# Performance work log

Measured on AMD Instinct MI355X. Metric: run time of the kernel, lower is better.

Reference implementation:

```python
import jax, jax.numpy as jnp
from jax import lax
import numpy as np

NUM_GRIDS = (40, 36, 24, 16, 12)
B, C = 4, 256
SMPL_OUT, CATE_OUT = 157, 1  # 24*6 pose + 10 shape + 3 cam; num_classes-1
SIZES = ((200, 200), (100, 100), (50, 50), (25, 25), (13, 13))


def setup_inputs():
    key = jax.random.key(0)
    ks = jax.random.split(key, 16)
    inp = {}
    for i, (h, w) in enumerate(SIZES):
        inp['feat%d' % i] = jax.random.normal(ks[i], (B, C, h, w), jnp.float32)
    def W(k, shape):
        return jax.random.normal(k, shape, jnp.float32) * 0.02
    inp['smpl_w0'] = W(ks[5], (C, C + 2, 3, 3)); inp['smpl_b0'] = jnp.zeros((C,), jnp.float32)
    inp['smpl_w'] = W(ks[6], (3, C, C, 3, 3)); inp['smpl_b'] = jnp.zeros((3, C), jnp.float32)
    inp['cate_w0'] = W(ks[7], (C, C, 3, 3)); inp['cate_b0'] = jnp.zeros((C,), jnp.float32)
    inp['cate_w'] = W(ks[8], (3, C, C, 3, 3)); inp['cate_b'] = jnp.zeros((3, C), jnp.float32)
    inp['cate_head_w'] = W(ks[9], (CATE_OUT, C, 3, 3)); inp['cate_head_b'] = jnp.zeros((CATE_OUT,), jnp.float32)
    inp['smpl_head_w'] = W(ks[10], (SMPL_OUT, C, 1, 1)); inp['smpl_head_b'] = jnp.zeros((SMPL_OUT,), jnp.float32)
    inp['smpl_init'] = W(ks[11], (SMPL_OUT,))  # stands in for init_contrep/shape/cam buffer
    return inp


def conv2d(x, w, b, pad):
    y = lax.conv_general_dilated(x, w, (1, 1), [(pad, pad), (pad, pad)],
                                 dimension_numbers=('NCHW', 'OIHW', 'NCHW'))
    return y + b[None, :, None, None]


def resize_ac(x, oh, ow):
    # bilinear resize, align_corners=True (matches F.interpolate(..., align_corners=True))
    H, W = x.shape[-2], x.shape[-1]
    ys = jnp.linspace(0.0, H - 1.0, oh)
    xs = jnp.linspace(0.0, W - 1.0, ow)
    y0 = jnp.floor(ys).astype(jnp.int32); y1 = jnp.minimum(y0 + 1, H - 1)
    x0 = jnp.floor(xs).astype(jnp.int32); x1 = jnp.minimum(x0 + 1, W - 1)
    wy = (ys - y0)[:, None]; wx = xs - x0
    r0, r1 = x[..., y0, :], x[..., y1, :]
    top = r0[..., x0] * (1 - wx) + r0[..., x1] * wx
    bot = r1[..., x0] * (1 - wx) + r1[..., x1] * wx
    return top * (1 - wy) + bot * wy


def points_nms(heat):
    # max_pool2d(kernel=2, stride=1, pad=1) -> (H+1, W+1); compare on [:-1, :-1]
    hmax = lax.reduce_window(heat, -jnp.inf, lax.max, (1, 1, 2, 2), (1, 1, 1, 1),
                             [(0, 0), (0, 0), (1, 1), (1, 1)])[:, :, :-1, :-1]
    return heat * (hmax == heat).astype(heat.dtype)


def _forward(feats, p):
    # split_feats: downsample P2 by 0.5, upsample P6 to P5 size (both align_corners bilinear)
    f0 = resize_ac(feats[0], feats[0].shape[-2] // 2, feats[0].shape[-1] // 2)
    f4 = resize_ac(feats[4], feats[3].shape[-2], feats[3].shape[-1])
    new_feats = (f0, feats[1], feats[2], feats[3], f4)
    smpl_outs, cate_outs = [], []
    for idx, x in enumerate(new_feats):
        g = NUM_GRIDS[idx]
        b, _, h, w = x.shape
        xr = jnp.linspace(-1.0, 1.0, w); yr = jnp.linspace(-1.0, 1.0, h)
        yy, xx = jnp.meshgrid(yr, xr, indexing='ij')
        coord = jnp.broadcast_to(jnp.stack([xx, yy])[None], (b, 2, h, w))  # CoordConv
        smpl_feat = resize_ac(jnp.concatenate([x, coord], axis=1), g, g)
        cate_feat = resize_ac(x, g, g)
        smpl_feat = jax.nn.relu(conv2d(smpl_feat, p['smpl_w0'], p['smpl_b0'], 1))
        cate_feat = jax.nn.relu(conv2d(cate_feat, p['cate_w0'], p['cate_b0'], 1))
        for i in range(3):  # remaining stacked convs (weights shared across levels)
            smpl_feat = jax.nn.relu(conv2d(smpl_feat, p['smpl_w'][i], p['smpl_b'][i], 1))
            cate_feat = jax.nn.relu(conv2d(cate_feat, p['cate_w'][i], p['cate_b'][i], 1))
        cate_pred = conv2d(cate_feat, p['cate_head_w'], p['cate_head_b'], 1)
        smpl_pred = conv2d(smpl_feat, p['smpl_head_w'], p['smpl_head_b'], 0) \
                    + p['smpl_init'][None, :, None, None]
        # eval=True branch: points-NMS on sigmoid heatmap, NHWC permute
        cate_pred = points_nms(jax.nn.sigmoid(cate_pred)).transpose(0, 2, 3, 1)
        smpl_pred = smpl_pred.transpose(0, 2, 3, 1)
        smpl_outs.append(smpl_pred); cate_outs.append(cate_pred)
    return tuple(smpl_outs) + tuple(cate_outs)


def reference(feat0, feat1, feat2, feat3, feat4, smpl_w0, smpl_b0, smpl_w, smpl_b,
              cate_w0, cate_b0, cate_w, cate_b, cate_head_w, cate_head_b,
              smpl_head_w, smpl_head_b, smpl_init):
    p = dict(smpl_w0=smpl_w0, smpl_b0=smpl_b0, smpl_w=smpl_w, smpl_b=smpl_b,
             cate_w0=cate_w0, cate_b0=cate_b0, cate_w=cate_w, cate_b=cate_b,
             cate_head_w=cate_head_w, cate_head_b=cate_head_b,
             smpl_head_w=smpl_head_w, smpl_head_b=smpl_head_b, smpl_init=smpl_init)
    return _forward((feat0, feat1, feat2, feat3, feat4), p)
```

## Files before the change

kernel.cpp:

```cpp
#include <hip/hip_runtime.h>
#include <math.h>
#include <stdint.h>

#define NLEV 5
#define PPT 17616
#define HPX 320

typedef __attribute__((ext_vector_type(8))) __bf16 bf16x8;
typedef __attribute__((ext_vector_type(4))) float f32x4;
typedef unsigned int u32;
typedef unsigned short u16;

#define MFMA16 __builtin_amdgcn_mfma_f32_16x16x32_bf16

__device__ __forceinline__ u32 f2bf(float f) {
  u32 u = __builtin_bit_cast(u32, f);
  return (u + 0x7FFFu + ((u >> 16) & 1u)) >> 16;
}
__device__ __forceinline__ void split2(float v, u32& hi, u32& lo) {
  hi = f2bf(v);
  lo = f2bf(v - __builtin_bit_cast(float, hi << 16));
}
__device__ __forceinline__ float bf2f(u32 bits16) {
  return __builtin_bit_cast(float, bits16 << 16);
}


struct PrepDesc {
  const float* src[9];
  int Cin[9];
  int Cout[9];
  int CB[9];
  int TAPS[9];
  int nCoT[9];
  int dstOff[9];
};

__global__ __launch_bounds__(256) void prep_weights(PrepDesc pd, u16* __restrict__ wHi,
                                                    u16* __restrict__ wLo) {
  int cfg = blockIdx.y;
  int CB = pd.CB[cfg];
  int TAPS = pd.TAPS[cfg];
  int KS = CB * TAPS;
  int total = KS * 2048 * pd.nCoT[cfg];
  int didx = blockIdx.x * 256 + threadIdx.x;
  if (didx >= total) return;
  int j = didx & 7;
  int lane = (didx >> 3) & 63;
  int wco = (didx >> 9) & 1;
  int f = (didx >> 10) & 1;
  int rest = didx >> 11;
  int ks = rest % KS;
  int coT = rest / KS;
  int cb = ks / TAPS;
  int tap = ks - cb * TAPS;
  int ci = cb * 32 + ((lane >> 4) << 3) + j;
  int co = coT * 64 + wco * 32 + f * 16 + (lane & 15);
  float v = 0.f;
  if (ci < pd.Cin[cfg] && co < pd.Cout[cfg])
    v = pd.src[cfg][((size_t)co * pd.Cin[cfg] + ci) * TAPS + tap];
  u32 hi, lo;
  split2(v, hi, lo);
  wHi[pd.dstOff[cfg] + didx] = (u16)hi;
  wLo[pd.dstOff[cfg] + didx] = (u16)lo;
}

struct ZeroDesc {
  int padOff[NLEV];
  int g[NLEV];
};

__global__ __launch_bounds__(256) void halo_zero(u16* __restrict__ base, ZeroDesc zd) {
  int px = blockIdx.x * 256 + threadIdx.x;
  if (px >= PPT) return;
  int l = 0;
#pragma unroll
  for (int i = 1; i < NLEV; i++)
    if (px >= zd.padOff[i]) l = i;
  int g = zd.g[l], gp2 = g + 2, hp2 = gp2 * gp2;
  int local = px - zd.padOff[l];
  int b = local / hp2;
  int rem = local - b * hp2;
  int yy = rem / gp2, xx = rem - yy * gp2;
  if (yy >= 1 && yy <= g && xx >= 1 && xx <= g) return;
  int r = blockIdx.y;
  uint4 z = {0u, 0u, 0u, 0u};
  *(uint4*)(base + ((size_t)r * PPT + px) * 8) = z;
}

struct BuildDesc {
  const float* src[NLEV];
  int H[NLEV];
  int mid[NLEV];
  int P[NLEV];
  int g[NLEV];
  int padOff[NLEV];
};

__device__ __forceinline__ float bsample(const float* __restrict__ pl, int H, int W,
                                         float fy, float fx) {
  int y0 = (int)floorf(fy);
  int y1 = min(y0 + 1, H - 1);
  float wy = fy - (float)y0;
  int x0 = (int)floorf(fx);
  int x1 = min(x0 + 1, W - 1);
  float wx = fx - (float)x0;
  const float* r0 = pl + (size_t)y0 * W;
  const float* r1 = pl + (size_t)y1 * W;
  float top = r0[x0] * (1.f - wx) + r0[x1] * wx;
  float bot = r1[x0] * (1.f - wx) + r1[x1] * wx;
  return top * (1.f - wy) + bot * wy;
}

__global__ __launch_bounds__(256) void build_all(BuildDesc bd, u16* __restrict__ dst) {
  int l = blockIdx.y;
  int P = bd.P[l];
  int g = bd.g[l];
  int total = 258 * P;
  int idx = blockIdx.x * 256 + threadIdx.x;
  if (idx >= total) return;
  int c = idx / P;
  int p = idx - c * P;
  int gg = g * g;
  int b = p / gg;
  int pr = p - b * gg;
  int i = pr / g;
  int j = pr - i * g;
  float val;
  if (c >= 256) {
    int tt = (c == 256) ? j : i;
    val = -1.f + 2.f * (float)tt / (float)(g - 1);
  } else {
    int H = bd.H[l], W = bd.H[l];
    int mid = bd.mid[l];
    const float* pl = bd.src[l] + ((size_t)b * 256 + c) * H * W;
    if (!mid) {
      float fy = (float)i * (float)(H - 1) / (float)(g - 1);
      float fx = (float)j * (float)(W - 1) / (float)(g - 1);
      val = bsample(pl, H, W, fy, fx);
    } else {
      int midh = mid, midw = mid;
      float fym = (float)i * (float)(midh - 1) / (float)(g - 1);
      float fxm = (float)j * (float)(midw - 1) / (float)(g - 1);
      int y0 = (int)floorf(fym);
      int y1 = min(y0 + 1, midh - 1);
      float wy = fym - (float)y0;
      int x0 = (int)floorf(fxm);
      int x1 = min(x0 + 1, midw - 1);
      float wx = fxm - (float)x0;
      float sy0 = (float)y0 * (float)(H - 1) / (float)(midh - 1);
      float sy1 = (float)y1 * (float)(H - 1) / (float)(midh - 1);
      float sx0 = (float)x0 * (float)(W - 1) / (float)(midw - 1);
      float sx1 = (float)x1 * (float)(W - 1) / (float)(midw - 1);
      float v00 = bsample(pl, H, W, sy0, sx0);
      float v01 = bsample(pl, H, W, sy0, sx1);
      float v10 = bsample(pl, H, W, sy1, sx0);
      float v11 = bsample(pl, H, W, sy1, sx1);
      float top = v00 * (1.f - wx) + v01 * wx;
      float bot = v10 * (1.f - wx) + v11 * wx;
      val = top * (1.f - wy) + bot * wy;
    }
  }
  int gp2 = g + 2;
  int hpos = bd.padOff[l] + b * gp2 * gp2 + (i + 1) * gp2 + (j + 1);
  u32 hi, lo;
  split2(val, hi, lo);
  size_t base = ((size_t)(c >> 3) * PPT + hpos) * 8 + (c & 7);
  dst[base] = (u16)hi;
  dst[(size_t)36 * PPT * 8 + base] = (u16)lo;
}

struct ConvDesc {
  int tS[NLEV + 1];
  int padOff[NLEV];
  int g[NLEV];
  int P[NLEV];
};

__global__ __launch_bounds__(256) void conv_mfma(
    const u16* __restrict__ inS, const u16* __restrict__ inC, int inRows,
    const u16* __restrict__ wHiB, const u16* __restrict__ wLoB, int wOffS,
    int wOffC, const float* __restrict__ bS, const float* __restrict__ bC,
    u16* __restrict__ outS, u16* __restrict__ outC, ConvDesc d, int CBS, int CBC) {
  const int bid = blockIdx.x;
  const int xcd = bid & 7;
  const int i6 = bid >> 3;
  const int tower = i6 & 1;
  const int coT = (i6 >> 1) & 3;
  const int tile = xcd + (i6 >> 3) * 8;
  if (tile >= d.tS[NLEV]) return;

  const u16* __restrict__ inHi = tower ? inC : inS;
  const u16* __restrict__ inLo = inHi + (size_t)inRows * PPT * 8;
  u16* __restrict__ outHi = tower ? outC : outS;
  u16* __restrict__ outLo = outHi + (size_t)32 * PPT * 8;
  const u16* __restrict__ wH = wHiB + (tower ? wOffC : wOffS);
  const u16* __restrict__ wL = wLoB + (tower ? wOffC : wOffS);
  const float* __restrict__ bias = tower ? bC : bS;
  const int CB = tower ? CBC : CBS;
  const int KS = CB * 9;

  int l = 0;
#pragma unroll
  for (int i = 1; i < NLEV; i++)
    if (tile >= d.tS[i]) l = i;
  const int g = d.g[l];
  const int gp2 = g + 2, hp2 = gp2 * gp2, gg = g * g;
  const int padOff = d.padOff[l];
  const int Pl = d.P[l];
  const int ptile = (tile - d.tS[l]) * 128;

  const int t = threadIdx.x;
  const int lane = t & 63;
  const int wv = t >> 6;
  const int wco = wv & 1, wp = wv >> 1;
  const int kb = lane >> 4;
  const int sgr = wv;

  int h0;
  {
    int b0 = ptile / gg, pr0 = ptile - b0 * gg;
    int y0 = pr0 / g, x0 = pr0 - y0 * g;
    h0 = padOff + b0 * hp2 + (y0 + 1) * gp2 + (x0 + 1) - gp2 - 1;
  }

  int hRel[4], ob[4];
  bool vst[4];
#pragma unroll
  for (int fi = 0; fi < 4; fi++) {
    int pb = ptile + wp * 64 + fi * 16;
    vst[fi] = pb < Pl;
    int pf = pb + (lane & 15);
    if (pf >= Pl) pf = Pl - 1;
    int b = pf / gg, pr = pf - b * gg;
    int y = pr / g, x = pr - y * g;
    int h = padOff + b * hp2 + (y + 1) * gp2 + (x + 1);
    hRel[fi] = h - h0;
    ob[fi] = h;
  }

  __shared__ u16 halo[2 * 4 * 2 * HPX * 8];

  f32x4 acc[2][4];
#pragma unroll
  for (int c = 0; c < 2; c++)
#pragma unroll
    for (int fi = 0; fi < 4; fi++) acc[c][fi] = (f32x4){0.f, 0.f, 0.f, 0.f};

  const size_t wbase =
      (size_t)coT * KS * 2048 + (size_t)wco * 512 + (size_t)lane * 8;
  bf16x8 ah0 = *(const bf16x8*)(wH + wbase);
  bf16x8 ah1 = *(const bf16x8*)(wH + wbase + 1024);
  bf16x8 al0 = *(const bf16x8*)(wL + wbase);
  bf16x8 al1 = *(const bf16x8*)(wL + wbase + 1024);

#define STAGE(dbuf, cbn)                                                          \
  {                                                                               \
    const int gr_ = (cbn)*4 + sgr;                                                \
    const u16* ghi_ = inHi + ((size_t)gr_ * PPT + h0) * 8;                        \
    const u16* glo_ = inLo + ((size_t)gr_ * PPT + h0) * 8;                        \
    u16* lb_ = halo + (size_t)(((dbuf)*4 + sgr) * 2) * (HPX * 8);                 \
    _Pragma("unroll") for (int i_ = 0; i_ < 5; i_++) {                            \
      __builtin_amdgcn_global_load_lds(                                           \
          (const __attribute__((address_space(1))) void*)(ghi_ +                  \
                                                          (size_t)(i_ * 64 + lane) * 8), \
          (__attribute__((address_space(3))) void*)(lb_ + i_ * 64 * 8), 16, 0, 0);\
      __builtin_amdgcn_global_load_lds(                                           \
          (const __attribute__((address_space(1))) void*)(glo_ +                  \
                                                          (size_t)(i_ * 64 + lane) * 8), \
          (__attribute__((address_space(3))) void*)(lb_ + HPX * 8 + i_ * 64 * 8), \
          16, 0, 0);                                                              \
    }                                                                             \
  }

  STAGE(0, 0);

  for (int cb = 0; cb < CB; ++cb) {
    const int cur = cb & 1;
    __syncthreads();
    if (cb + 1 < CB) STAGE(cur ^ 1, cb + 1);

#pragma unroll
    for (int tap = 0; tap < 9; ++tap) {
      const int ks = cb * 9 + tap;
      bf16x8 ah0n, ah1n, al0n, al1n;
      const bool have = (ks + 1) < KS;
      if (have) {
        size_t wo = wbase + (size_t)(ks + 1) * 2048;
        ah0n = *(const bf16x8*)(wH + wo);
        ah1n = *(const bf16x8*)(wH + wo + 1024);
        al0n = *(const bf16x8*)(wL + wo);
        al1n = *(const bf16x8*)(wL + wo + 1024);
      }
      const int toff = (tap / 3 - 1) * gp2 + (tap % 3) - 1;
      const u16* kbase = halo + (size_t)((cur * 4 + kb) * 2) * (HPX * 8);
#pragma unroll
      for (int fi = 0; fi < 4; fi++) {
        const u16* p0 = kbase + (hRel[fi] + toff) * 8;
        bf16x8 bh = *(const bf16x8*)p0;
        bf16x8 bl = *(const bf16x8*)(p0 + HPX * 8);
        acc[0][fi] = MFMA16(ah0, bh, acc[0][fi], 0, 0, 0);
        acc[0][fi] = MFMA16(ah0, bl, acc[0][fi], 0, 0, 0);
        acc[0][fi] = MFMA16(al0, bh, acc[0][fi], 0, 0, 0);
        acc[1][fi] = MFMA16(ah1, bh, acc[1][fi], 0, 0, 0);
        acc[1][fi] = MFMA16(ah1, bl, acc[1][fi], 0, 0, 0);
        acc[1][fi] = MFMA16(al1, bh, acc[1][fi], 0, 0, 0);
      }
      if (have) {
        ah0 = ah0n;
        ah1 = ah1n;
        al0 = al0n;
        al1 = al1n;
      }
    }
  }
#undef STAGE

  const int coBase = coT * 64 + wco * 32 + ((lane >> 4) << 2);
  float bAv[4], bBv[4];
#pragma unroll
  for (int i = 0; i < 4; i++) {
    bAv[i] = bias[coBase + i];
    bBv[i] = bias[coBase + 16 + i];
  }
  const size_t rowA = (size_t)(coBase >> 3) * PPT;
  const size_t rowB = (size_t)((coBase + 16) >> 3) * PPT;
  const int sub = coBase & 7;
#pragma unroll
  for (int fi = 0; fi < 4; fi++) {
    if (!vst[fi]) continue;
    u32 h[4], lo[4];
#pragma unroll
    for (int i = 0; i < 4; i++)
      split2(fmaxf(acc[0][fi][i] + bAv[i], 0.f), h[i], lo[i]);
    uint2 hs = {h[0] | (h[1] << 16), h[2] | (h[3] << 16)};
    uint2 ls = {lo[0] | (lo[1] << 16), lo[2] | (lo[3] << 16)};
    *(uint2*)(outHi + (rowA + ob[fi]) * 8 + sub) = hs;
    *(uint2*)(outLo + (rowA + ob[fi]) * 8 + sub) = ls;
#pragma unroll
    for (int i = 0; i < 4; i++)
      split2(fmaxf(acc[1][fi][i] + bBv[i], 0.f), h[i], lo[i]);
    hs.x = h[0] | (h[1] << 16);
    hs.y = h[2] | (h[3] << 16);
    ls.x = lo[0] | (lo[1] << 16);
    ls.y = lo[2] | (lo[3] << 16);
    *(uint2*)(outHi + (rowB + ob[fi]) * 8 + sub) = hs;
    *(uint2*)(outLo + (rowB + ob[fi]) * 8 + sub) = ls;
  }
}

struct HeadDesc {
  int tS64[NLEV + 1];
  int padOff[NLEV];
  int g[NLEV];
  int outOff[NLEV];
};

__global__ __launch_bounds__(256) void head1x1(
    const u16* __restrict__ inHi, const u16* __restrict__ inLo,
    const u16* __restrict__ wH, const u16* __restrict__ wL,
    const float* __restrict__ bias, const float* __restrict__ bias2,
    float* __restrict__ outB, HeadDesc d) {
  const int bx = blockIdx.x;
  const int coT = blockIdx.y;
  int l = 0;
#pragma unroll
  for (int i = 1; i < NLEV; i++)
    if (bx >= d.tS64[i]) l = i;
  const int g = d.g[l], gp2 = g + 2, hp2 = gp2 * gp2, gg = g * g;
  const int ptile = (bx - d.tS64[l]) * 64;
  const int t = threadIdx.x, lane = t & 63, wv = t >> 6;
  const int wco = wv & 1, wp = wv >> 1, kb = lane >> 4;

  int hp[2], pF[2];
#pragma unroll
  for (int fi = 0; fi < 2; fi++) {
    int pf = ptile + wp * 32 + fi * 16 + (lane & 15);
    pF[fi] = pf;
    int b = pf / gg, pr = pf - b * gg, y = pr / g, x = pr - y * g;
    hp[fi] = d.padOff[l] + b * hp2 + (y + 1) * gp2 + (x + 1);
  }
  f32x4 acc[2][2];
#pragma unroll
  for (int c = 0; c < 2; c++)
#pragma unroll
    for (int fi = 0; fi < 2; fi++) acc[c][fi] = (f32x4){0.f, 0.f, 0.f, 0.f};

  const size_t wbase = (size_t)coT * 8 * 2048 + (size_t)wco * 512 + (size_t)lane * 8;
  for (int cb = 0; cb < 8; ++cb) {
    size_t wo = wbase + (size_t)cb * 2048;
    bf16x8 ah0 = *(const bf16x8*)(wH + wo);
    bf16x8 ah1 = *(const bf16x8*)(wH + wo + 1024);
    bf16x8 al0 = *(const bf16x8*)(wL + wo);
    bf16x8 al1 = *(const bf16x8*)(wL + wo + 1024);
    const int gr = cb * 4 + kb;
#pragma unroll
    for (int fi = 0; fi < 2; fi++) {
      bf16x8 bh = *(const bf16x8*)(inHi + ((size_t)gr * PPT + hp[fi]) * 8);
      bf16x8 bl = *(const bf16x8*)(inLo + ((size_t)gr * PPT + hp[fi]) * 8);
      acc[0][fi] = MFMA16(ah0, bh, acc[0][fi], 0, 0, 0);
      acc[0][fi] = MFMA16(ah0, bl, acc[0][fi], 0, 0, 0);
      acc[0][fi] = MFMA16(al0, bh, acc[0][fi], 0, 0, 0);
      acc[1][fi] = MFMA16(ah1, bh, acc[1][fi], 0, 0, 0);
      acc[1][fi] = MFMA16(ah1, bl, acc[1][fi], 0, 0, 0);
      acc[1][fi] = MFMA16(al1, bh, acc[1][fi], 0, 0, 0);
    }
  }
  const int coBase = coT * 64 + wco * 32 + ((lane >> 4) << 2);
#pragma unroll
  for (int c = 0; c < 2; c++)
#pragma unroll
    for (int fi = 0; fi < 2; fi++)
#pragma unroll
      for (int i = 0; i < 4; i++) {
        int co = coBase + c * 16 + i;
        if (co < 157)
          outB[d.outOff[l] + (size_t)pF[fi] * 157 + co] =
              acc[c][fi][i] + bias[co] + bias2[co];
      }
}

struct CHDesc {
  int tS64[NLEV + 1];
  int padOff[NLEV];
  int g[NLEV];
  int outOff[NLEV];
};

__global__ __launch_bounds__(256) void cate_head_all(
    const u16* __restrict__ inHi, const u16* __restrict__ inLo,
    const float* __restrict__ w, const float* __restrict__ bias,
    float* __restrict__ heat, CHDesc d) {
  int tile = blockIdx.x;
  int l = 0;
#pragma unroll
  for (int i = 1; i < NLEV; i++)
    if (tile >= d.tS64[i]) l = i;
  const int g = d.g[l];
  const int gp2 = g + 2, hp2 = gp2 * gp2, gg = g * g;
  const int t = threadIdx.x;
  const int ps = t & 63;
  const int cw = t >> 6;
  const int ptile = (tile - d.tS64[l]) * 64;
  int p = ptile + ps;
  int b = p / gg, pr = p - b * gg, y = pr / g, x = pr - y * g;
  const int hbase = d.padOff[l] + b * hp2 + (y + 1) * gp2 + (x + 1);

  __shared__ float ws[32][9][8];
  for (int i = t; i < 2304; i += 256) {
    int ci = i / 9, tap = i - ci * 9;
    ws[ci >> 3][tap][ci & 7] = w[i];
  }
  __syncthreads();

  float s = 0.f;
  for (int gr = cw; gr < 32; gr += 4) {
    const u16* ph = inHi + ((size_t)gr * PPT + hbase) * 8;
    const u16* pl = inLo + ((size_t)gr * PPT + hbase) * 8;
#pragma unroll
    for (int tap = 0; tap < 9; tap++) {
      const int toff = (tap / 3 - 1) * gp2 + (tap % 3) - 1;
      uint4 hq = *(const uint4*)(ph + (ptrdiff_t)toff * 8);
      uint4 lq = *(const uint4*)(pl + (ptrdiff_t)toff * 8);
      const float* wp = ws[gr][tap];
      s += (bf2f(hq.x & 0xFFFFu) + bf2f(lq.x & 0xFFFFu)) * wp[0] +
           (bf2f(hq.x >> 16) + bf2f(lq.x >> 16)) * wp[1] +
           (bf2f(hq.y & 0xFFFFu) + bf2f(lq.y & 0xFFFFu)) * wp[2] +
           (bf2f(hq.y >> 16) + bf2f(lq.y >> 16)) * wp[3] +
           (bf2f(hq.z & 0xFFFFu) + bf2f(lq.z & 0xFFFFu)) * wp[4] +
           (bf2f(hq.z >> 16) + bf2f(lq.z >> 16)) * wp[5] +
           (bf2f(hq.w & 0xFFFFu) + bf2f(lq.w & 0xFFFFu)) * wp[6] +
           (bf2f(hq.w >> 16) + bf2f(lq.w >> 16)) * wp[7];
    }
  }
  __shared__ float red[4][64];
  red[cw][ps] = s;
  __syncthreads();
  if (cw == 0) {
    float tot = bias[0] + red[0][ps] + red[1][ps] + red[2][ps] + red[3][ps];
    heat[d.outOff[l] + p] = 1.f / (1.f + expf(-tot));
  }
}

struct SmallDesc {
  int P[NLEV];
  int g[NLEV];
  int inOff[NLEV];
  int outOff[NLEV];
};

__global__ void nms_all(const float* __restrict__ heat, float* __restrict__ out,
                        SmallDesc d) {
  int l = blockIdx.y;
  int P = d.P[l], g = d.g[l];
  int gg = g * g;
  int p = blockIdx.x * 256 + threadIdx.x;
  if (p >= P) return;
  int pr = p % gg;
  int y = pr / g;
  int x = pr - y * g;
  const float* hb = heat + d.inOff[l];
  float c = hb[p], m = c;
  if (y > 0) {
    m = fmaxf(m, hb[p - g]);
    if (x > 0) m = fmaxf(m, hb[p - g - 1]);
  }
  if (x > 0) m = fmaxf(m, hb[p - 1]);
  out[d.outOff[l] + p] = (m == c) ? c : 0.f;
}

extern "C" void kernel_launch(void* const* d_in, const int* in_sizes, int n_in,
                              void* d_out, int out_size, void* d_ws, size_t ws_size,
                              hipStream_t stream) {
  const float* feat[5];
  for (int i = 0; i < 5; i++) feat[i] = (const float*)d_in[i];
  const float* smpl_w0 = (const float*)d_in[5];
  const float* smpl_b0 = (const float*)d_in[6];
  const float* smpl_w = (const float*)d_in[7];
  const float* smpl_b = (const float*)d_in[8];
  const float* cate_w0 = (const float*)d_in[9];
  const float* cate_b0 = (const float*)d_in[10];
  const float* cate_w = (const float*)d_in[11];
  const float* cate_b = (const float*)d_in[12];
  const float* cate_head_w = (const float*)d_in[13];
  const float* cate_head_b = (const float*)d_in[14];
  const float* smpl_head_w = (const float*)d_in[15];
  const float* smpl_head_b = (const float*)d_in[16];
  const float* smpl_init = (const float*)d_in[17];
  float* out = (float*)d_out;

  static const int GR[5] = {40, 36, 24, 16, 12};
  static const int SH[5] = {200, 100, 50, 25, 13};
  static const int MIDW[5] = {100, 0, 0, 0, 25};

  int P[5], cumP[6], tS64[6], tS128[6], padOff[5];
  cumP[0] = 0;
  tS64[0] = 0;
  tS128[0] = 0;
  int po = 0;
  for (int l = 0; l < 5; l++) {
    P[l] = 4 * GR[l] * GR[l];
    cumP[l + 1] = cumP[l] + P[l];
    tS64[l + 1] = tS64[l] + P[l] / 64;
    tS128[l + 1] = tS128[l] + (P[l] + 127) / 128;
    padOff[l] = po;
    po += 4 * (GR[l] + 2) * (GR[l] + 2);
  }

  int smpl_off[5], cate_off[5];
  {
    int off = 0;
    for (int l = 0; l < 5; l++) {
      smpl_off[l] = off;
      off += P[l] * 157;
    }
    for (int l = 0; l < 5; l++) {
      cate_off[l] = off;
      off += P[l];
    }
  }

  u16* bufA = (u16*)d_ws;
  u16* bufBs = bufA + (size_t)72 * PPT * 8;
  u16* bufCs = bufBs + (size_t)64 * PPT * 8;
  u16* bufBc = bufCs + (size_t)64 * PPT * 8;
  u16* bufCc = bufBc + (size_t)64 * PPT * 8;
  float* heat = (float*)(bufCc + (size_t)64 * PPT * 8);
  u16* wHi = (u16*)(heat + 15488);

  PrepDesc pd;
  const size_t LSTR = (size_t)256 * 256 * 9;
  pd.src[0] = smpl_w0;
  pd.src[1] = smpl_w;
  pd.src[2] = smpl_w + LSTR;
  pd.src[3] = smpl_w + 2 * LSTR;
  pd.src[4] = cate_w0;
  pd.src[5] = cate_w;
  pd.src[6] = cate_w + LSTR;
  pd.src[7] = cate_w + 2 * LSTR;
  pd.src[8] = smpl_head_w;
  for (int i = 0; i < 9; i++) {
    pd.Cin[i] = 256;
    pd.Cout[i] = 256;
    pd.CB[i] = 8;
    pd.TAPS[i] = 9;
    pd.nCoT[i] = 4;
  }
  pd.Cin[0] = 258;
  pd.CB[0] = 9;
  pd.Cout[8] = 157;
  pd.TAPS[8] = 1;
  pd.nCoT[8] = 3;
  size_t WTOT = 0;
  for (int i = 0; i < 9; i++) {
    pd.dstOff[i] = (int)WTOT;
    WTOT += (size_t)pd.CB[i] * pd.TAPS[i] * 2048 * pd.nCoT[i];
  }
  u16* wLo = wHi + WTOT;

  hipMemsetAsync(bufA, 0, (size_t)36 * PPT * 32, stream);
  ZeroDesc zd;
  for (int l = 0; l < 5; l++) {
    zd.padOff[l] = padOff[l];
    zd.g[l] = GR[l];
  }
  hipLaunchKernelGGL(halo_zero, dim3((PPT + 255) / 256, 256), dim3(256), 0, stream,
                     bufBs, zd);

  hipLaunchKernelGGL(prep_weights, dim3(2592, 9), dim3(256), 0, stream, pd, wHi, wLo);

  BuildDesc bd;
  for (int l = 0; l < 5; l++) {
    bd.src[l] = feat[l];
    bd.H[l] = SH[l];
    bd.mid[l] = MIDW[l];
    bd.P[l] = P[l];
    bd.g[l] = GR[l];
    bd.padOff[l] = padOff[l];
  }
  hipLaunchKernelGGL(build_all, dim3((258 * P[0] + 255) / 256, 5), dim3(256), 0,
                     stream, bd, bufA);

  ConvDesc cd;
  HeadDesc hd;
  CHDesc chd;
  SmallDesc nd;
  for (int i = 0; i <= 5; i++) {
    cd.tS[i] = tS128[i];
    hd.tS64[i] = tS64[i];
    chd.tS64[i] = tS64[i];
  }
  for (int l = 0; l < 5; l++) {
    cd.padOff[l] = padOff[l];
    cd.g[l] = GR[l];
    cd.P[l] = P[l];
    hd.padOff[l] = padOff[l];
    hd.g[l] = GR[l];
    hd.outOff[l] = smpl_off[l];
    chd.padOff[l] = padOff[l];
    chd.g[l] = GR[l];
    chd.outOff[l] = cumP[l];
    nd.P[l] = P[l];
    nd.g[l] = GR[l];
    nd.inOff[l] = cumP[l];
    nd.outOff[l] = cate_off[l];
  }

  const int NT64 = tS64[5];
  const int CGRID = 8 * 128;
  hipLaunchKernelGGL(conv_mfma, dim3(CGRID), dim3(256), 0, stream, bufA, bufA, 36,
                     wHi, wLo, pd.dstOff[0], pd.dstOff[4], smpl_b0, cate_b0, bufBs,
                     bufBc, cd, 9, 8);
  hipLaunchKernelGGL(conv_mfma, dim3(CGRID), dim3(256), 0, stream, bufBs, bufBc, 32,
                     wHi, wLo, pd.dstOff[1], pd.dstOff[5], smpl_b + 0, cate_b + 0,
                     bufCs, bufCc, cd, 8, 8);
  hipLaunchKernelGGL(conv_mfma, dim3(CGRID), dim3(256), 0, stream, bufCs, bufCc, 32,
                     wHi, wLo, pd.dstOff[2], pd.dstOff[6], smpl_b + 256,
                     cate_b + 256, bufBs, bufBc, cd, 8, 8);
  hipLaunchKernelGGL(conv_mfma, dim3(CGRID), dim3(256), 0, stream, bufBs, bufBc, 32,
                     wHi, wLo, pd.dstOff[3], pd.dstOff[7], smpl_b + 512,
                     cate_b + 512, bufCs, bufCc, cd, 8, 8);
  hipLaunchKernelGGL(head1x1, dim3(NT64, 3), dim3(256), 0, stream, bufCs,
                     bufCs + (size_t)32 * PPT * 8, wHi + pd.dstOff[8],
                     wLo + pd.dstOff[8], smpl_head_b, smpl_init, out, hd);
  hipLaunchKernelGGL(cate_head_all, dim3(NT64), dim3(256), 0, stream, bufCc,
                     bufCc + (size_t)32 * PPT * 8, cate_head_w, cate_head_b, heat,
                     chd);
  hipLaunchKernelGGL(nms_all, dim3((P[0] + 255) / 256, 5), dim3(256), 0, stream,
                     heat, out, nd);
  (void)in_sizes;
  (void)n_in;
  (void)out_size;
  (void)ws_size;
}
```

Baseline: 506.9 us.

## Drop activation low-part split for smpl tower, keep split only for cate tower

The smpl tower now stores its activations as a single bf16 term instead of a hi/lo pair. Its conv blocks skip the low-part halo load and two of the six MFMAs per fragment, and the 1x1 head reads one activation buffer. The buffer layout and halo zeroing are shrunk to match. This lowers memory traffic and MFMA work for half the conv blocks, at the cost of reduced activation precision in the smpl branch. The two towers also become imbalanced in work within the same launch.

Result: no change. 500.6 us, median of 2 (-1.2%).

```diff
diff --git a/kernel.cpp b/kernel.cpp
--- a/kernel.cpp
+++ b/kernel.cpp
@@ -178,7 +178,7 @@
 };
 
 __global__ __launch_bounds__(256) void conv_mfma(
-    const u16* __restrict__ inS, const u16* __restrict__ inC, int inRows,
+    const u16* __restrict__ inS, const u16* __restrict__ inC, int inCRows,
     const u16* __restrict__ wHiB, const u16* __restrict__ wLoB, int wOffS,
     int wOffC, const float* __restrict__ bS, const float* __restrict__ bC,
     u16* __restrict__ outS, u16* __restrict__ outC, ConvDesc d, int CBS, int CBC) {
@@ -190,8 +190,9 @@
   const int tile = xcd + (i6 >> 3) * 8;
   if (tile >= d.tS[NLEV]) return;
 
+  const bool dual = (tower != 0);
   const u16* __restrict__ inHi = tower ? inC : inS;
-  const u16* __restrict__ inLo = inHi + (size_t)inRows * PPT * 8;
+  const u16* __restrict__ inLo = inHi + (size_t)inCRows * PPT * 8;
   u16* __restrict__ outHi = tower ? outC : outS;
   u16* __restrict__ outLo = outHi + (size_t)32 * PPT * 8;
   const u16* __restrict__ wH = wHiB + (tower ? wOffC : wOffS);
@@ -258,18 +259,23 @@
   {                                                                               \
     const int gr_ = (cbn)*4 + sgr;                                                \
     const u16* ghi_ = inHi + ((size_t)gr_ * PPT + h0) * 8;                        \
-    const u16* glo_ = inLo + ((size_t)gr_ * PPT + h0) * 8;                        \
     u16* lb_ = halo + (size_t)(((dbuf)*4 + sgr) * 2) * (HPX * 8);                 \
     _Pragma("unroll") for (int i_ = 0; i_ < 5; i_++) {                            \
       __builtin_amdgcn_global_load_lds(                                           \
           (const __attribute__((address_space(1))) void*)(ghi_ +                  \
                                                           (size_t)(i_ * 64 + lane) * 8), \
           (__attribute__((address_space(3))) void*)(lb_ + i_ * 64 * 8), 16, 0, 0);\
-      __builtin_amdgcn_global_load_lds(                                           \
-          (const __attribute__((address_space(1))) void*)(glo_ +                  \
-                                                          (size_t)(i_ * 64 + lane) * 8), \
-          (__attribute__((address_space(3))) void*)(lb_ + HPX * 8 + i_ * 64 * 8), \
-          16, 0, 0);                                                              \
+    }                                                                             \
+    if (dual) {                                                                   \
+      const u16* glo_ = inLo + ((size_t)gr_ * PPT + h0) * 8;                      \
+      _Pragma("unroll") for (int i_ = 0; i_ < 5; i_++) {                          \
+        __builtin_amdgcn_global_load_lds(                                         \
+            (const __attribute__((address_space(1))) void*)(glo_ +                \
+                                                            (size_t)(i_ * 64 + lane) * 8), \
+            (__attribute__((address_space(3))) void*)(lb_ + HPX * 8 +             \
+                                                      i_ * 64 * 8),               \
+            16, 0, 0);                                                            \
+      }                                                                           \
     }                                                                             \
   }
 
@@ -298,13 +304,15 @@
       for (int fi = 0; fi < 4; fi++) {
         const u16* p0 = kbase + (hRel[fi] + toff) * 8;
         bf16x8 bh = *(const bf16x8*)p0;
-        bf16x8 bl = *(const bf16x8*)(p0 + HPX * 8);
         acc[0][fi] = MFMA16(ah0, bh, acc[0][fi], 0, 0, 0);
-        acc[0][fi] = MFMA16(ah0, bl, acc[0][fi], 0, 0, 0);
         acc[0][fi] = MFMA16(al0, bh, acc[0][fi], 0, 0, 0);
         acc[1][fi] = MFMA16(ah1, bh, acc[1][fi], 0, 0, 0);
-        acc[1][fi] = MFMA16(ah1, bl, acc[1][fi], 0, 0, 0);
         acc[1][fi] = MFMA16(al1, bh, acc[1][fi], 0, 0, 0);
+        if (dual) {
+          bf16x8 bl = *(const bf16x8*)(p0 + HPX * 8);
+          acc[0][fi] = MFMA16(ah0, bl, acc[0][fi], 0, 0, 0);
+          acc[1][fi] = MFMA16(ah1, bl, acc[1][fi], 0, 0, 0);
+        }
       }
       if (have) {
         ah0 = ah0n;
@@ -329,23 +337,36 @@
 #pragma unroll
   for (int fi = 0; fi < 4; fi++) {
     if (!vst[fi]) continue;
-    u32 h[4], lo[4];
-#pragma unroll
-    for (int i = 0; i < 4; i++)
-      split2(fmaxf(acc[0][fi][i] + bAv[i], 0.f), h[i], lo[i]);
-    uint2 hs = {h[0] | (h[1] << 16), h[2] | (h[3] << 16)};
-    uint2 ls = {lo[0] | (lo[1] << 16), lo[2] | (lo[3] << 16)};
-    *(uint2*)(outHi + (rowA + ob[fi]) * 8 + sub) = hs;
-    *(uint2*)(outLo + (rowA + ob[fi]) * 8 + sub) = ls;
-#pragma unroll
-    for (int i = 0; i < 4; i++)
-      split2(fmaxf(acc[1][fi][i] + bBv[i], 0.f), h[i], lo[i]);
-    hs.x = h[0] | (h[1] << 16);
-    hs.y = h[2] | (h[3] << 16);
-    ls.x = lo[0] | (lo[1] << 16);
-    ls.y = lo[2] | (lo[3] << 16);
-    *(uint2*)(outHi + (rowB + ob[fi]) * 8 + sub) = hs;
-    *(uint2*)(outLo + (rowB + ob[fi]) * 8 + sub) = ls;
+    if (!dual) {
+      u32 h[4];
+#pragma unroll
+      for (int i = 0; i < 4; i++) h[i] = f2bf(fmaxf(acc[0][fi][i] + bAv[i], 0.f));
+      uint2 hs = {h[0] | (h[1] << 16), h[2] | (h[3] << 16)};
+      *(uint2*)(outHi + (rowA + ob[fi]) * 8 + sub) = hs;
+#pragma unroll
+      for (int i = 0; i < 4; i++) h[i] = f2bf(fmaxf(acc[1][fi][i] + bBv[i], 0.f));
+      hs.x = h[0] | (h[1] << 16);
+      hs.y = h[2] | (h[3] << 16);
+      *(uint2*)(outHi + (rowB + ob[fi]) * 8 + sub) = hs;
+    } else {
+      u32 h[4], lo[4];
+#pragma unroll
+      for (int i = 0; i < 4; i++)
+        split2(fmaxf(acc[0][fi][i] + bAv[i], 0.f), h[i], lo[i]);
+      uint2 hs = {h[0] | (h[1] << 16), h[2] | (h[3] << 16)};
+      uint2 ls = {lo[0] | (lo[1] << 16), lo[2] | (lo[3] << 16)};
+      *(uint2*)(outHi + (rowA + ob[fi]) * 8 + sub) = hs;
+      *(uint2*)(outLo + (rowA + ob[fi]) * 8 + sub) = ls;
+#pragma unroll
+      for (int i = 0; i < 4; i++)
+        split2(fmaxf(acc[1][fi][i] + bBv[i], 0.f), h[i], lo[i]);
+      hs.x = h[0] | (h[1] << 16);
+      hs.y = h[2] | (h[3] << 16);
+      ls.x = lo[0] | (lo[1] << 16);
+      ls.y = lo[2] | (lo[3] << 16);
+      *(uint2*)(outHi + (rowB + ob[fi]) * 8 + sub) = hs;
+      *(uint2*)(outLo + (rowB + ob[fi]) * 8 + sub) = ls;
+    }
   }
 }
 
@@ -357,10 +378,9 @@
 };
 
 __global__ __launch_bounds__(256) void head1x1(
-    const u16* __restrict__ inHi, const u16* __restrict__ inLo,
-    const u16* __restrict__ wH, const u16* __restrict__ wL,
-    const float* __restrict__ bias, const float* __restrict__ bias2,
-    float* __restrict__ outB, HeadDesc d) {
+    const u16* __restrict__ actIn, const u16* __restrict__ wH,
+    const u16* __restrict__ wL, const float* __restrict__ bias,
+    const float* __restrict__ bias2, float* __restrict__ outB, HeadDesc d) {
   const int bx = blockIdx.x;
   const int coT = blockIdx.y;
   int l = 0;
@@ -396,14 +416,11 @@
     const int gr = cb * 4 + kb;
 #pragma unroll
     for (int fi = 0; fi < 2; fi++) {
-      bf16x8 bh = *(const bf16x8*)(inHi + ((size_t)gr * PPT + hp[fi]) * 8);
-      bf16x8 bl = *(const bf16x8*)(inLo + ((size_t)gr * PPT + hp[fi]) * 8);
-      acc[0][fi] = MFMA16(ah0, bh, acc[0][fi], 0, 0, 0);
-      acc[0][fi] = MFMA16(ah0, bl, acc[0][fi], 0, 0, 0);
-      acc[0][fi] = MFMA16(al0, bh, acc[0][fi], 0, 0, 0);
-      acc[1][fi] = MFMA16(ah1, bh, acc[1][fi], 0, 0, 0);
-      acc[1][fi] = MFMA16(ah1, bl, acc[1][fi], 0, 0, 0);
-      acc[1][fi] = MFMA16(al1, bh, acc[1][fi], 0, 0, 0);
+      bf16x8 b = *(const bf16x8*)(actIn + ((size_t)gr * PPT + hp[fi]) * 8);
+      acc[0][fi] = MFMA16(ah0, b, acc[0][fi], 0, 0, 0);
+      acc[0][fi] = MFMA16(al0, b, acc[0][fi], 0, 0, 0);
+      acc[1][fi] = MFMA16(ah1, b, acc[1][fi], 0, 0, 0);
+      acc[1][fi] = MFMA16(al1, b, acc[1][fi], 0, 0, 0);
     }
   }
   const int coBase = coT * 64 + wco * 32 + ((lane >> 4) << 2);
@@ -562,8 +579,8 @@
 
   u16* bufA = (u16*)d_ws;
   u16* bufBs = bufA + (size_t)72 * PPT * 8;
-  u16* bufCs = bufBs + (size_t)64 * PPT * 8;
-  u16* bufBc = bufCs + (size_t)64 * PPT * 8;
+  u16* bufCs = bufBs + (size_t)32 * PPT * 8;
+  u16* bufBc = bufCs + (size_t)32 * PPT * 8;
   u16* bufCc = bufBc + (size_t)64 * PPT * 8;
   float* heat = (float*)(bufCc + (size_t)64 * PPT * 8);
   u16* wHi = (u16*)(heat + 15488);
@@ -598,13 +615,13 @@
   }
   u16* wLo = wHi + WTOT;
 
-  hipMemsetAsync(bufA, 0, (size_t)36 * PPT * 32, stream);
+  hipMemsetAsync(bufA, 0, (size_t)72 * PPT * 16, stream);
   ZeroDesc zd;
   for (int l = 0; l < 5; l++) {
     zd.padOff[l] = padOff[l];
     zd.g[l] = GR[l];
   }
-  hipLaunchKernelGGL(halo_zero, dim3((PPT + 255) / 256, 256), dim3(256), 0, stream,
+  hipLaunchKernelGGL(halo_zero, dim3((PPT + 255) / 256, 192), dim3(256), 0, stream,
                      bufBs, zd);
 
   hipLaunchKernelGGL(prep_weights, dim3(2592, 9), dim3(256), 0, stream, pd, wHi, wLo);
@@ -661,8 +678,8 @@
                      wHi, wLo, pd.dstOff[3], pd.dstOff[7], smpl_b + 512,
                      cate_b + 512, bufCs, bufCc, cd, 8, 8);
   hipLaunchKernelGGL(head1x1, dim3(NT64, 3), dim3(256), 0, stream, bufCs,
-                     bufCs + (size_t)32 * PPT * 8, wHi + pd.dstOff[8],
-                     wLo + pd.dstOff[8], smpl_head_b, smpl_init, out, hd);
+                     wHi + pd.dstOff[8], wLo + pd.dstOff[8], smpl_head_b, smpl_init,
+                     out, hd);
   hipLaunchKernelGGL(cate_head_all, dim3(NT64), dim3(256), 0, stream, bufCc,
                      bufCc + (size_t)32 * PPT * 8, cate_head_w, cate_head_b, heat,
                      chd);
```
